# Kernel tuning notes

Hardware: AMD Instinct MI355X
Metric: run time of the kernel (lower is better)

The kernel has to match this reference:

```python
import jax, jax.numpy as jnp
import numpy as np

LN_EPS = 1e-5

def setup_inputs() -> dict:
    key = jax.random.key(0)
    k1, k2, k3, k4 = jax.random.split(key, 4)
    B, N, D, E = 2, 50000, 128, 800000
    H = jax.random.normal(k1, (B, N, D), dtype=jnp.float32)
    src = jax.random.randint(k2, (E,), 0, N, dtype=jnp.int64)
    dst = jax.random.randint(k3, (E,), 0, N, dtype=jnp.int64)
    W = jax.random.normal(k4, (D, D), dtype=jnp.float32) * (1.0 / np.sqrt(D))
    gamma = jnp.ones((D,), dtype=jnp.float32)
    beta = jnp.zeros((D,), dtype=jnp.float32)
    return {"H": H, "src": src, "dst": dst, "W": W, "gamma": gamma, "beta": beta}

def reference(H, src, dst, W, gamma, beta):
    # m = Linear(H) (no bias): [B,N,D]
    m = jnp.einsum('bnd,de->bne', H, W)
    # gather messages at src, scatter-add into dst along node dim
    agg = jnp.zeros_like(m).at[:, dst, :].add(m[:, src, :])
    x = H + jax.nn.gelu(agg, approximate=False)
    # LayerNorm over last dim
    mu = jnp.mean(x, axis=-1, keepdims=True)
    var = jnp.var(x, axis=-1, keepdims=True)
    return (x - mu) * jax.lax.rsqrt(var + LN_EPS) * gamma + beta
```

## Files before the change

kernel.cpp:

```cpp
#include <hip/hip_runtime.h>
#include <math.h>

#define DIM 128
#define LN_EPS 1e-5f
#define CAP 64
#define WT_STRIDE 136

typedef unsigned short bf16_t;
typedef unsigned short u16;
typedef __attribute__((ext_vector_type(8))) short bf16x8;
typedef __attribute__((ext_vector_type(4))) float f32x4;

__device__ __forceinline__ bf16_t f2bf(float f) {
    unsigned u = __builtin_bit_cast(unsigned, f);
    u += 0x7FFFu + ((u >> 16) & 1u);
    return (bf16_t)(u >> 16);
}
__device__ __forceinline__ float bf2f(bf16_t h) {
    unsigned u = ((unsigned)h) << 16;
    return __builtin_bit_cast(float, u);
}

__global__ __launch_bounds__(256) void gemm_fill_kernel(
    const float* __restrict__ Hmat, const float* __restrict__ W,
    bf16_t* __restrict__ Mout,
    const int* __restrict__ src, const int* __restrict__ dst,
    int* __restrict__ cursor, u16* __restrict__ eidxT,
    int nrows, int N, int E, int FB)
{
    __shared__ bf16_t sWT[DIM * WT_STRIDE];

    if ((int)blockIdx.x < FB) {
        int e = blockIdx.x * 256 + threadIdx.x;
        if (e < E) {
            int d = dst[e];
            int pos = atomicAdd(&cursor[d], 1);
            if (pos < CAP) eidxT[(size_t)pos * N + d] = (u16)src[e];
        }
        return;
    }

    const int tid = threadIdx.x;
    const int gblock = blockIdx.x - FB;

    {
        const float4* W4 = (const float4*)W;
        #pragma unroll
        for (int i = 0; i < 16; ++i) {
            int idx4 = i * 256 + tid;
            int k  = idx4 >> 5;
            int n0 = (idx4 & 31) * 4;
            float4 w = W4[idx4];
            sWT[(n0 + 0) * WT_STRIDE + k] = f2bf(w.x);
            sWT[(n0 + 1) * WT_STRIDE + k] = f2bf(w.y);
            sWT[(n0 + 2) * WT_STRIDE + k] = f2bf(w.z);
            sWT[(n0 + 3) * WT_STRIDE + k] = f2bf(w.w);
        }
    }
    __syncthreads();

    const int wave = tid >> 6;
    const int lane = tid & 63;
    const int quad = lane >> 4;
    const int l15  = lane & 15;

    const int arow = gblock * 64 + wave * 16 + l15;
    const float* Arow = Hmat + (size_t)((arow < nrows) ? arow : 0) * DIM;

    f32x4 acc[8];
    #pragma unroll
    for (int t = 0; t < 8; ++t) acc[t] = (f32x4){0.f, 0.f, 0.f, 0.f};

    #pragma unroll
    for (int ks = 0; ks < 4; ++ks) {
        const int k0 = ks * 32 + quad * 8;
        float4 a0 = *(const float4*)&Arow[k0];
        float4 a1 = *(const float4*)&Arow[k0 + 4];
        bf16x8 af;
        af[0] = (short)f2bf(a0.x); af[1] = (short)f2bf(a0.y);
        af[2] = (short)f2bf(a0.z); af[3] = (short)f2bf(a0.w);
        af[4] = (short)f2bf(a1.x); af[5] = (short)f2bf(a1.y);
        af[6] = (short)f2bf(a1.z); af[7] = (short)f2bf(a1.w);

        #pragma unroll
        for (int t = 0; t < 8; ++t) {
            bf16x8 bf = *(const bf16x8*)&sWT[(t * 16 + l15) * WT_STRIDE + k0];
            acc[t] = __builtin_amdgcn_mfma_f32_16x16x32_bf16(af, bf, acc[t], 0, 0, 0);
        }
    }

    const int outrowbase = gblock * 64 + wave * 16 + quad * 4;
    #pragma unroll
    for (int r = 0; r < 4; ++r) {
        int rr = outrowbase + r;
        if (rr < nrows) {
            int b = (rr >= N) ? 1 : 0;
            int n = rr - (b ? N : 0);
            bf16_t* orow = Mout + ((size_t)n * 2 + b) * DIM + l15;
            #pragma unroll
            for (int t = 0; t < 8; ++t)
                orow[t * 16] = f2bf(acc[t][r]);
        }
    }
}

__global__ __launch_bounds__(256) void gather_kernel(
    const bf16_t* __restrict__ M, const float* __restrict__ Hmat,
    const int* __restrict__ cursor, const u16* __restrict__ eidxT,
    const float* __restrict__ gamma, const float* __restrict__ beta,
    float* __restrict__ out, int N)
{
    const int wave = threadIdx.x >> 6;
    const int lane = threadIdx.x & 63;
    const int node = blockIdx.x * 4 + wave;
    if (node >= N) return;

    const int b  = lane >> 5;
    const int c4 = lane & 31;

    int cnt = cursor[node];
    if (cnt > CAP) cnt = CAP;

    int myidx = (lane < cnt) ? (int)eidxT[(size_t)lane * N + node] : 0;

    const ushort4* M4 = (const ushort4*)M;

    float acc0 = 0.f, acc1 = 0.f, acc2 = 0.f, acc3 = 0.f;
    int j = 0;
    for (; j + 8 <= cnt; j += 8) {
        ushort4 v[8];
        #pragma unroll
        for (int q = 0; q < 8; ++q) {
            int s = __shfl(myidx, j + q, 64);
            v[q] = M4[(size_t)s * 64 + lane];
        }
        #pragma unroll
        for (int q = 0; q < 8; ++q) {
            acc0 += bf2f(v[q].x); acc1 += bf2f(v[q].y);
            acc2 += bf2f(v[q].z); acc3 += bf2f(v[q].w);
        }
    }
    for (; j < cnt; ++j) {
        int s = __shfl(myidx, j, 64);
        ushort4 v0 = M4[(size_t)s * 64 + lane];
        acc0 += bf2f(v0.x); acc1 += bf2f(v0.y);
        acc2 += bf2f(v0.z); acc3 += bf2f(v0.w);
    }

    const size_t elembase = ((size_t)b * N + node) * DIM + c4 * 4;
    float4 h = *(const float4*)&Hmat[elembase];
    const float inv_sqrt2 = 0.70710678118654752f;
    float x0 = h.x + 0.5f * acc0 * (1.f + erff(acc0 * inv_sqrt2));
    float x1 = h.y + 0.5f * acc1 * (1.f + erff(acc1 * inv_sqrt2));
    float x2 = h.z + 0.5f * acc2 * (1.f + erff(acc2 * inv_sqrt2));
    float x3 = h.w + 0.5f * acc3 * (1.f + erff(acc3 * inv_sqrt2));

    float s  = x0 + x1 + x2 + x3;
    float ss = x0 * x0 + x1 * x1 + x2 * x2 + x3 * x3;
    #pragma unroll
    for (int o = 16; o > 0; o >>= 1) {
        s  += __shfl_xor(s,  o, 64);
        ss += __shfl_xor(ss, o, 64);
    }
    const float mean = s * (1.f / DIM);
    const float var  = ss * (1.f / DIM) - mean * mean;
    const float inv  = rsqrtf(var + LN_EPS);

    float4 gm = *(const float4*)&gamma[c4 * 4];
    float4 bt = *(const float4*)&beta[c4 * 4];
    float4 o;
    o.x = (x0 - mean) * inv * gm.x + bt.x;
    o.y = (x1 - mean) * inv * gm.y + bt.y;
    o.z = (x2 - mean) * inv * gm.z + bt.z;
    o.w = (x3 - mean) * inv * gm.w + bt.w;
    *(float4*)&out[elembase] = o;
}

extern "C" void kernel_launch(void* const* d_in, const int* in_sizes, int n_in,
                              void* d_out, int out_size, void* d_ws, size_t ws_size,
                              hipStream_t stream)
{
    const float* H     = (const float*)d_in[0];
    const int*   src   = (const int*)  d_in[1];
    const int*   dst   = (const int*)  d_in[2];
    const float* W     = (const float*)d_in[3];
    const float* gamma = (const float*)d_in[4];
    const float* beta  = (const float*)d_in[5];
    float* out = (float*)d_out;

    const int E     = in_sizes[1];
    const int total = in_sizes[0];
    const int nrows = total / DIM;
    const int N     = nrows / 2;

    char* ws = (char*)d_ws;
    bf16_t* Mbuf = (bf16_t*)ws;   ws += (size_t)total * sizeof(bf16_t);
    int* cursor  = (int*)ws;      ws += (size_t)N * sizeof(int);
    u16* eidxT   = (u16*)ws;      ws += (size_t)CAP * N * sizeof(u16);

    hipMemsetAsync(cursor, 0, (size_t)N * sizeof(int), stream);

    const int FB = (E + 255) / 256;
    const int GB = (nrows + 63) / 64;

    gemm_fill_kernel<<<FB + GB, 256, 0, stream>>>(H, W, Mbuf, src, dst,
                                                  cursor, eidxT, nrows, N, E, FB);

    gather_kernel<<<(N + 3) / 4, 256, 0, stream>>>(Mbuf, H, cursor, eidxT,
                                                   gamma, beta, out, N);
}
```

Baseline: 227.3 us.

## Pretranspose W once in prep kernel, drop per-block LDS staging, batch edge fill

A new prep kernel converts and transposes W to bf16 once in global memory and zeroes the cursor array, replacing the hipMemsetAsync call. The GEMM blocks no longer stage W into LDS or synchronise, and instead read B fragments straight from global/L2. The fill blocks each handle 8 edges per thread, with loads issued before the atomics. This removes redundant per-block W conversion and the LDS footprint, which may raise occupancy. In exchange it adds a kernel launch and relies on cache hits for the repeated W reads.

```diff
diff --git a/kernel.cpp b/kernel.cpp
--- a/kernel.cpp
+++ b/kernel.cpp
@@ -4,7 +4,7 @@
 #define DIM 128
 #define LN_EPS 1e-5f
 #define CAP 64
-#define WT_STRIDE 136
+#define EPT 8
 
 typedef unsigned short bf16_t;
 typedef unsigned short u16;
@@ -21,44 +21,54 @@
     return __builtin_bit_cast(float, u);
 }
 
+__global__ __launch_bounds__(256) void prep_kernel(
+    const float* __restrict__ W, bf16_t* __restrict__ WT,
+    int* __restrict__ cursor, int N)
+{
+    if (blockIdx.x < 16) {
+        int i = blockIdx.x * 256 + threadIdx.x;
+        float4 w = ((const float4*)W)[i];
+        int k  = i >> 5;
+        int n0 = (i & 31) * 4;
+        WT[(n0 + 0) * DIM + k] = f2bf(w.x);
+        WT[(n0 + 1) * DIM + k] = f2bf(w.y);
+        WT[(n0 + 2) * DIM + k] = f2bf(w.z);
+        WT[(n0 + 3) * DIM + k] = f2bf(w.w);
+    } else {
+        int i = (blockIdx.x - 16) * 256 + threadIdx.x;
+        if (i < N) cursor[i] = 0;
+    }
+}
+
 __global__ __launch_bounds__(256) void gemm_fill_kernel(
-    const float* __restrict__ Hmat, const float* __restrict__ W,
+    const float* __restrict__ Hmat, const bf16_t* __restrict__ WT,
     bf16_t* __restrict__ Mout,
     const int* __restrict__ src, const int* __restrict__ dst,
     int* __restrict__ cursor, u16* __restrict__ eidxT,
     int nrows, int N, int E, int FB)
 {
-    __shared__ bf16_t sWT[DIM * WT_STRIDE];
-
     if ((int)blockIdx.x < FB) {
-        int e = blockIdx.x * 256 + threadIdx.x;
-        if (e < E) {
-            int d = dst[e];
-            int pos = atomicAdd(&cursor[d], 1);
-            if (pos < CAP) eidxT[(size_t)pos * N + d] = (u16)src[e];
+        const int base = blockIdx.x * (256 * EPT) + threadIdx.x;
+        int d[EPT], s[EPT];
+        #pragma unroll
+        for (int i = 0; i < EPT; ++i) {
+            int e = base + i * 256;
+            bool ok = (e < E);
+            d[i] = ok ? dst[e] : -1;
+            s[i] = ok ? src[e] : 0;
+        }
+        #pragma unroll
+        for (int i = 0; i < EPT; ++i) {
+            if (d[i] >= 0) {
+                int pos = atomicAdd(&cursor[d[i]], 1);
+                if (pos < CAP) eidxT[(size_t)pos * N + d[i]] = (u16)s[i];
+            }
         }
         return;
     }
 
     const int tid = threadIdx.x;
     const int gblock = blockIdx.x - FB;
-
-    {
-        const float4* W4 = (const float4*)W;
-        #pragma unroll
-        for (int i = 0; i < 16; ++i) {
-            int idx4 = i * 256 + tid;
-            int k  = idx4 >> 5;
-            int n0 = (idx4 & 31) * 4;
-            float4 w = W4[idx4];
-            sWT[(n0 + 0) * WT_STRIDE + k] = f2bf(w.x);
-            sWT[(n0 + 1) * WT_STRIDE + k] = f2bf(w.y);
-            sWT[(n0 + 2) * WT_STRIDE + k] = f2bf(w.z);
-            sWT[(n0 + 3) * WT_STRIDE + k] = f2bf(w.w);
-        }
-    }
-    __syncthreads();
-
     const int wave = tid >> 6;
     const int lane = tid & 63;
     const int quad = lane >> 4;
@@ -84,7 +94,7 @@
 
         #pragma unroll
         for (int t = 0; t < 8; ++t) {
-            bf16x8 bf = *(const bf16x8*)&sWT[(t * 16 + l15) * WT_STRIDE + k0];
+            bf16x8 bf = *(const bf16x8*)&WT[(t * 16 + l15) * DIM + k0];
             acc[t] = __builtin_amdgcn_mfma_f32_16x16x32_bf16(af, bf, acc[t], 0, 0, 0);
         }
     }
@@ -197,13 +207,14 @@
     bf16_t* Mbuf = (bf16_t*)ws;   ws += (size_t)total * sizeof(bf16_t);
     int* cursor  = (int*)ws;      ws += (size_t)N * sizeof(int);
     u16* eidxT   = (u16*)ws;      ws += (size_t)CAP * N * sizeof(u16);
-
-    hipMemsetAsync(cursor, 0, (size_t)N * sizeof(int), stream);
-
-    const int FB = (E + 255) / 256;
+    bf16_t* WT   = (bf16_t*)ws;   ws += (size_t)DIM * DIM * sizeof(bf16_t);
+
+    prep_kernel<<<16 + (N + 255) / 256, 256, 0, stream>>>(W, WT, cursor, N);
+
+    const int FB = (E + 256 * EPT - 1) / (256 * EPT);
     const int GB = (nrows + 63) / 64;
 
-    gemm_fill_kernel<<<FB + GB, 256, 0, stream>>>(H, W, Mbuf, src, dst,
+    gemm_fill_kernel<<<FB + GB, 256, 0, stream>>>(H, WT, Mbuf, src, dst,
                                                   cursor, eidxT, nrows, N, E, FB);
 
     gather_kernel<<<(N + 3) / 4, 256, 0, stream>>>(Mbuf, H, cursor, eidxT,
```

Measured after the change: 227.6 us. Within noise of the previous version (+0.1%).
